# Kernel optimization log

Hardware: AMD Instinct MI355X
Metric: run time of the kernel (lower is better)

## Reference

```python
import jax, jax.numpy as jnp
import numpy as np
from jax import lax

B, T, D = 256, 512, 256          # batch, time, input_dim (neurons)
HE, HC, HG = 256, 256, 256       # encoder/controller/generator hidden
L, F = 64, 64                    # latent_dim, factor_dim


def gru_cell(x, h, Wih, Whh, bih, bhh):
    # PyTorch GRU gate order: r, z, n
    gi = x @ Wih.T + bih
    gh = h @ Whh.T + bhh
    ir, iz, inn = jnp.split(gi, 3, axis=-1)
    hr, hz, hn = jnp.split(gh, 3, axis=-1)
    r = jax.nn.sigmoid(ir + hr)
    z = jax.nn.sigmoid(iz + hz)
    n = jnp.tanh(inn + r * hn)
    return (1.0 - z) * n + z * h


def setup_inputs() -> dict:
    key = jax.random.key(0)
    ks = iter(jax.random.split(key, 40))
    def p(shape, scale=0.05):
        return (jax.random.normal(next(ks), shape, dtype=jnp.float32) * scale)
    inp = {
        "x": jax.random.normal(next(ks), (B, T, D), dtype=jnp.float32),
        "eps_u": jax.random.normal(next(ks), (T, B, L), dtype=jnp.float32),
        # bidirectional encoder GRU (forward / backward directions)
        "Wih_ef": p((3 * HE, D)), "Whh_ef": p((3 * HE, HE)), "bih_ef": p((3 * HE,)), "bhh_ef": p((3 * HE,)),
        "Wih_eb": p((3 * HE, D)), "Whh_eb": p((3 * HE, HE)), "bih_eb": p((3 * HE,)), "bhh_eb": p((3 * HE,)),
        # initial-condition heads
        "W_mu0": p((L, 2 * HE)), "b_mu0": p((L,)), "W_lv0": p((L, 2 * HE)), "b_lv0": p((L,)),
        # controller GRU + heads
        "Wih_c": p((3 * HC, D + F)), "Whh_c": p((3 * HC, HC)), "bih_c": p((3 * HC,)), "bhh_c": p((3 * HC,)),
        "W_cmu": p((L, HC)), "b_cmu": p((L,)), "W_clv": p((L, HC)), "b_clv": p((L,)),
        # generator GRU
        "Wih_g": p((3 * HG, L)), "Whh_g": p((3 * HG, HG)), "bih_g": p((3 * HG,)), "bhh_g": p((3 * HG,)),
        # readouts
        "W_f": p((F, HG)), "b_f": p((F,)), "W_r": p((D, F)), "b_r": p((D,)),
    }
    return inp


def reference(x, eps_u, Wih_ef, Whh_ef, bih_ef, bhh_ef, Wih_eb, Whh_eb, bih_eb, bhh_eb,
              W_mu0, b_mu0, W_lv0, b_lv0, Wih_c, Whh_c, bih_c, bhh_c,
              W_cmu, b_cmu, W_clv, b_clv, Wih_g, Whh_g, bih_g, bhh_g,
              W_f, b_f, W_r, b_r):
    xt = jnp.transpose(x, (1, 0, 2))  # [T, B, D]
    h0 = jnp.zeros((x.shape[0], HE), dtype=x.dtype)

    def enc_f(h, x_t):
        return gru_cell(x_t, h, Wih_ef, Whh_ef, bih_ef, bhh_ef), None

    def enc_b(h, x_t):
        return gru_cell(x_t, h, Wih_eb, Whh_eb, bih_eb, bhh_eb), None

    h_fwd, _ = lax.scan(enc_f, h0, xt)
    h_bwd, _ = lax.scan(enc_b, h0, xt, reverse=True)
    h_enc = jnp.concatenate([h_fwd, h_bwd], axis=-1)  # [B, 2*HE]

    mu0 = h_enc @ W_mu0.T + b_mu0
    lv0 = h_enc @ W_lv0.T + b_lv0
    kl_ics = (0.5 * jnp.sum(jnp.exp(lv0) + mu0 ** 2 - 1.0 - lv0, axis=1)).mean()
    # note: z0 is sampled in the original but never used (generator starts from zeros)

    c0 = jnp.zeros((x.shape[0], HC), dtype=x.dtype)
    g0 = jnp.zeros((x.shape[0], HG), dtype=x.dtype)
    f0 = jnp.zeros((x.shape[0], F), dtype=x.dtype)

    def step(carry, inputs):
        c_h, g_h, prev_f = carry
        x_t, eps_t = inputs
        c_in = jnp.concatenate([x_t, prev_f], axis=-1)  # [B, D+F]
        c_h = gru_cell(c_in, c_h, Wih_c, Whh_c, bih_c, bhh_c)
        mu_u = c_h @ W_cmu.T + b_cmu
        lv_u = c_h @ W_clv.T + b_clv
        u_t = mu_u + eps_t * jnp.exp(0.5 * lv_u)
        kl_t = (0.5 * jnp.sum(jnp.exp(lv_u) + mu_u ** 2 - 1.0 - lv_u, axis=1)).mean()
        g_h = gru_cell(u_t, g_h, Wih_g, Whh_g, bih_g, bhh_g)
        factors = g_h @ W_f.T + b_f
        rates_t = jnp.exp(factors @ W_r.T + b_r)
        return (c_h, g_h, factors), (rates_t, factors, kl_t)

    _, (rates, factors_all, kl_ts) = lax.scan(step, (c0, g0, f0), (xt, eps_u))
    rates = jnp.transpose(rates, (1, 0, 2))           # [B, T, D]
    factors_all = jnp.transpose(factors_all, (1, 0, 2))  # [B, T, F]
    kl_ctrl = kl_ts.mean()  # sum of per-step means / T
    return (rates, kl_ics, kl_ctrl, factors_all)
```

## Files before the change

### kernel.cpp

```cpp
#include <hip/hip_runtime.h>

typedef unsigned char u8;
typedef unsigned short u16;
typedef unsigned int u32;
typedef unsigned long long u64;
typedef short short8 __attribute__((ext_vector_type(8)));
typedef __bf16 bf16x8 __attribute__((ext_vector_type(8)));
typedef float f32x4 __attribute__((ext_vector_type(4)));
typedef float f32x2 __attribute__((ext_vector_type(2)));
typedef long longx2 __attribute__((ext_vector_type(2)));

#define DEV static __device__ __forceinline__

struct Params {
  const float *x, *eps;
  const float *Wih_ef, *Whh_ef, *bih_ef, *bhh_ef;
  const float *Wih_eb, *Whh_eb, *bih_eb, *bhh_eb;
  const float *W_mu0, *b_mu0, *W_lv0, *b_lv0;
  const float *Wih_c, *Whh_c, *bih_c, *bhh_c;
  const float *W_cmu, *b_cmu, *W_clv, *b_clv;
  const float *Wih_g, *Whh_g, *bih_g, *bhh_g;
  const float *W_f, *b_f, *W_r, *b_r;
  u8  *Xf8;
  u16 *ebf;
  u16 *wihcbf;
  float *bfc;
  u8 *wihef8, *whhef8, *wiheb8, *whheb8;
  u8 *whhc8, *whhg8;
  u8 *wihcf8, *wihg8;
  u8 *wf8, *wcmu8, *wclv8;
  u16 *wrbf;
  float *cbn;
  float *gb;
  float *hdb;
  float *fb2;
  float *eb;
  float *henc;
  float *klacc;
  float *klics;
  u8 *Gxc;
  float *out;
};

constexpr size_t RATES_N = 33554432ull;
constexpr size_t FOUT    = RATES_N + 2ull;

DEV u16 f2bf(float x) {
  unsigned u = __builtin_bit_cast(unsigned, x);
  u = (u + 0x7FFFu + ((u >> 16) & 1u)) >> 16;
  return (u16)u;
}
DEV float bf2f(u32 s) { return __builtin_bit_cast(float, s << 16); }
DEV unsigned f2e4m3(float x) {
  unsigned u = __builtin_bit_cast(unsigned, x);
  unsigned s = (u >> 24) & 0x80u;
  float ax = __builtin_bit_cast(float, u & 0x7FFFFFFFu);
  if (ax > 448.f) return s | 0x7E;
  if (ax < 0.0009765625f) return s;
  if (ax < 0.015625f) {
    int m = (int)rintf(ax * 512.f);
    if (m >= 8) return s | 0x08;
    return s | (unsigned)m;
  }
  unsigned au = __builtin_bit_cast(unsigned, ax);
  int E = (int)(au >> 23) - 127;
  unsigned m = au & 0x7FFFFFu;
  unsigned r = (m + 0x7FFFFu + ((m >> 20) & 1u)) >> 20;
  if (r >= 8) { r = 0; ++E; if (E > 8) return s | 0x7E; }
  return s | ((unsigned)(E + 7) << 3) | r;
}
DEV float e4m3tof(unsigned b) {
  unsigned s = (b & 0x80u) << 24;
  unsigned e = (b >> 3) & 15u, m = b & 7u;
  float v;
  if (e) v = __builtin_bit_cast(float, ((e + 120u) << 23) | (m << 20));
  else   v = (float)m * 0.001953125f;
  return __builtin_bit_cast(float, __builtin_bit_cast(unsigned, v) | s);
}
template <bool HI>
DEV unsigned pk2fp8(float a, float b, unsigned old) {
#if __has_builtin(__builtin_amdgcn_cvt_pk_fp8_f32)
  return (unsigned)__builtin_amdgcn_cvt_pk_fp8_f32(a, b, (int)old, HI);
#else
  unsigned p = f2e4m3(a) | (f2e4m3(b) << 8);
  return HI ? ((old & 0xFFFFu) | (p << 16)) : ((old & 0xFFFF0000u) | p);
#endif
}
template <bool HI>
DEV f32x2 pkf32(unsigned w) {
#if __has_builtin(__builtin_amdgcn_cvt_pk_f32_fp8)
  return __builtin_amdgcn_cvt_pk_f32_fp8((int)w, HI);
#else
  unsigned h = HI ? (w >> 16) : w;
  f32x2 r; r[0] = e4m3tof(h & 255u); r[1] = e4m3tof((h >> 8) & 255u); return r;
#endif
}
DEV float sigm(float x) { return 1.f / (1.f + __expf(-x)); }
DEV float ftanh(float x) { float t = __expf(2.f * x); return 1.f - 2.f / (t + 1.f); }
DEV float gru_h(float pr, float pz, float pin, float phn, float hp) {
  float r = sigm(pr), z = sigm(pz);
  float n = ftanh(pin + r * phn);
  return (1.f - z) * n + z * hp;
}
DEV u64 pack8f8(const float* s) {
  u64 p = 0;
  #pragma unroll
  for (int e = 0; e < 8; ++e) p |= (u64)f2e4m3(s[e]) << (8 * e);
  return p;
}

DEV f32x4 MFMA(short8 a, short8 b, f32x4 c) {
  return __builtin_amdgcn_mfma_f32_16x16x32_bf16(
      __builtin_bit_cast(bf16x8, a), __builtin_bit_cast(bf16x8, b), c, 0, 0, 0);
}
DEV f32x4 mfma8(long a, long b, f32x4 c) {
  return __builtin_amdgcn_mfma_f32_16x16x32_fp8_fp8(a, b, c, 0, 0, 0);
}
DEV short8 ldfrag(const u16* p0, int stride) {
  const int l = threadIdx.x & 63;
  const u16* p = p0 + (size_t)(l & 15) * stride + ((l >> 4) << 3);
  return *reinterpret_cast<const short8*>(p);
}
DEV short8 ldfrag_f32(const float* p0, int stride) {
  const int l = threadIdx.x & 63;
  const float* p = p0 + (size_t)(l & 15) * stride + ((l >> 4) << 3);
  f32x4 a = *reinterpret_cast<const f32x4*>(p);
  f32x4 b = *reinterpret_cast<const f32x4*>(p + 4);
  short8 r;
  r[0]=(short)f2bf(a[0]); r[1]=(short)f2bf(a[1]); r[2]=(short)f2bf(a[2]); r[3]=(short)f2bf(a[3]);
  r[4]=(short)f2bf(b[0]); r[5]=(short)f2bf(b[1]); r[6]=(short)f2bf(b[2]); r[7]=(short)f2bf(b[3]);
  return r;
}
DEV longx2 ldws2(const u8* w, int tile, int p) {
  return *(const longx2*)(w + ((size_t)tile << 12) + (p << 10) + ((threadIdx.x & 63) << 4));
}
DEV longx2 ldws64x(const u8* w, int tile) {
  return *(const longx2*)(w + ((size_t)tile << 10) + ((threadIdx.x & 63) << 4));
}
DEV int fragoff(int row, int jb) { return jb * 128 + ((row ^ (jb & 15)) << 3); }
DEV long ldsF(const u8* m, int r0, int rs, int kk) {
  int l = threadIdx.x & 63;
  int jb = kk * 4 + (l >> 4);
  return *(const long*)(m + ((r0 >> 4) << (rs + 4)) + fragoff(l & 15, jb));
}
DEV void stF(u8* m, int row, int col, unsigned v) {
  *(unsigned*)(m + fragoff(row, col >> 3) + (col & 7)) = v;
}
DEV short8 ldsB16(const u8* m, int r0, int kk) {
  int l = threadIdx.x & 63;
  int row = r0 + (l & 15);
  int off = row * 512 + kk * 64 + ((l >> 4) << 4);
  off ^= (row & 7) << 4;
  return *(const short8*)(m + off);
}
DEV void stage16(u8* dst, const u8* src, int nbytes) {
  for (int i = threadIdx.x * 16; i < nbytes; i += blockDim.x * 16) {
    int row = i >> 9;
    int off = i ^ ((row & 7) << 4);
    *(f32x4*)(dst + off) = *(const f32x4*)(src + i);
  }
}

__global__ __launch_bounds__(256) void k_init(Params P) {
  const size_t g  = (size_t)blockIdx.x * 256 + threadIdx.x;
  const size_t gs = (size_t)gridDim.x * 256;
  for (size_t i = g; i < 4194304ull; i += gs) {
    size_t flat = i << 3;
    int b = (int)(flat >> 17);
    int rem = (int)(flat & 131071);
    int t = rem >> 8, d = rem & 255;
    *(u64*)(P.Xf8 + (((size_t)t * 256 + b) << 8) + d) = pack8f8(P.x + flat);
  }
  for (size_t o = g; o < 1048576ull; o += gs) {
    int l = (int)(o & 63), k2 = (int)((o >> 6) & 1);
    int bt = (int)((o >> 7) & 15), t = (int)(o >> 11);
    int row = bt * 16 + (l & 15), col = k2 * 32 + ((l >> 4) << 3);
    const float* s = P.eps + ((size_t)t * 256 + row) * 64 + col;
    f32x4 v0 = *(const f32x4*)s, v1 = *(const f32x4*)(s + 4);
    short8 ob;
    ob[0]=(short)f2bf(v0[0]); ob[1]=(short)f2bf(v0[1]); ob[2]=(short)f2bf(v0[2]); ob[3]=(short)f2bf(v0[3]);
    ob[4]=(short)f2bf(v1[0]); ob[5]=(short)f2bf(v1[1]); ob[6]=(short)f2bf(v1[2]); ob[7]=(short)f2bf(v1[3]);
    *(short8*)((u8*)P.ebf + o * 16) = ob;
  }
  const int gi = (int)g, gsi = (int)gs;
  for (int i = gi; i < 24576; i += gsi) {
    int l = i & 63, kk = (i >> 6) & 7, tile = i >> 9;
    int row = tile * 16 + (l & 15), col = kk * 32 + ((l >> 4) << 3);
    size_t so = (size_t)row * 256 + col;
    size_t db = ((size_t)tile << 12) + ((kk >> 1) << 10) + (l << 4) + ((kk & 1) << 3);
    *(u64*)(P.whhc8  + db) = pack8f8(P.Whh_c  + so);
    *(u64*)(P.whhg8  + db) = pack8f8(P.Whh_g  + so);
    *(u64*)(P.wihef8 + db) = pack8f8(P.Wih_ef + so);
    *(u64*)(P.whhef8 + db) = pack8f8(P.Whh_ef + so);
    *(u64*)(P.wiheb8 + db) = pack8f8(P.Wih_eb + so);
    *(u64*)(P.whheb8 + db) = pack8f8(P.Whh_eb + so);
  }
  for (int i = gi; i < 2048; i += gsi) {
    int l = i & 63, kk = (i >> 6) & 7, tile = i >> 9;
    int row = tile * 16 + (l & 15), col = kk * 32 + ((l >> 4) << 3);
    size_t so = (size_t)row * 256 + col;
    size_t db = ((size_t)tile << 12) + ((kk >> 1) << 10) + (l << 4) + ((kk & 1) << 3);
    *(u64*)(P.wf8   + db) = pack8f8(P.W_f   + so);
    *(u64*)(P.wcmu8 + db) = pack8f8(P.W_cmu + so);
    *(u64*)(P.wclv8 + db) = pack8f8(P.W_clv + so);
  }
  for (int i = gi; i < 6144; i += gsi) {
    int l = i & 63, k2 = (i >> 6) & 1, tile = i >> 7;
    int row = tile * 16 + (l & 15), col = k2 * 32 + ((l >> 4) << 3);
    size_t db = ((size_t)tile << 10) + (l << 4) + (k2 << 3);
    *(u64*)(P.wihcf8 + db) = pack8f8(P.Wih_c + (size_t)row * 320 + 256 + col);
    *(u64*)(P.wihg8  + db) = pack8f8(P.Wih_g + (size_t)row * 64 + col);
  }
  for (int i = gi; i < 196608; i += gsi) {
    int r = i >> 8, c = i & 255;
    P.wihcbf[i] = f2bf(P.Wih_c[r * 320 + c]);
  }
  for (int i = gi; i < 16384; i += gsi) P.wrbf[i] = f2bf(P.W_r[i]);
  for (int i = gi; i < 768; i += gsi)
    P.bfc[i] = P.bih_c[i] + (i < 512 ? P.bhh_c[i] : 0.f);
  for (int i = gi; i < 256; i += gsi) {
    P.cbn[i] = P.bhh_c[512 + i];
    P.gb[i]        = P.bih_g[i] + P.bhh_g[i];
    P.gb[256 + i]  = P.bih_g[256 + i] + P.bhh_g[256 + i];
    P.gb[512 + i]  = P.bih_g[512 + i];
    P.gb[768 + i]  = P.bhh_g[512 + i];
    P.eb[i]        = P.bih_ef[i] + P.bhh_ef[i];
    P.eb[256 + i]  = P.bih_ef[256 + i] + P.bhh_ef[256 + i];
    P.eb[512 + i]  = P.bih_ef[512 + i];
    P.eb[768 + i]  = P.bhh_ef[512 + i];
    P.eb[1024 + i] = P.bih_eb[i] + P.bhh_eb[i];
    P.eb[1280 + i] = P.bih_eb[256 + i] + P.bhh_eb[256 + i];
    P.eb[1536 + i] = P.bih_eb[512 + i];
    P.eb[1792 + i] = P.bhh_eb[512 + i];
  }
  for (int i = gi; i < 128; i += gsi) P.hdb[i] = (i < 64) ? P.b_cmu[i] : P.b_clv[i - 64];
  for (int i = gi; i < 64; i += gsi)  P.fb2[i] = P.b_f[i];
}

__global__ __launch_bounds__(512, 2) void k_gx(Params P) {
  extern __shared__ char smem[];
  u8* sA = (u8*)smem;
  u8* sB = sA + 65536;
  const int nc = blockIdx.x % 6;
  const int tb = blockIdx.x / 6;
  const int t = tb >> 1, bh = tb & 1;
  stage16(sA, (const u8*)(P.wihcbf + (size_t)nc * 128 * 256), 65536);
  for (int i = threadIdx.x * 8; i < 32768; i += 512 * 8) {
    int r = i >> 8, c = i & 255;
    const float* s = P.x + ((size_t)(bh * 128 + r) * 512 + t) * 256 + c;
    f32x4 v0 = *(const f32x4*)s, v1 = *(const f32x4*)(s + 4);
    short8 o;
    o[0]=(short)f2bf(v0[0]); o[1]=(short)f2bf(v0[1]); o[2]=(short)f2bf(v0[2]); o[3]=(short)f2bf(v0[3]);
    o[4]=(short)f2bf(v1[0]); o[5]=(short)f2bf(v1[1]); o[6]=(short)f2bf(v1[2]); o[7]=(short)f2bf(v1[3]);
    int off = (r * 512 + c * 2) ^ ((r & 7) << 4);
    *(short8*)(sB + off) = o;
  }
  __syncthreads();
  const int lane = threadIdx.x & 63, wid = threadIdx.x >> 6;
  const int rq = (lane >> 4) << 2;
  const int nglob = nc * 128 + wid * 16;
  short8 Af[8];
  #pragma unroll
  for (int kk = 0; kk < 8; ++kk) Af[kk] = ldsB16(sA, wid * 16, kk);
  float bq[4];
  #pragma unroll
  for (int q = 0; q < 4; ++q) bq[q] = P.bfc[nglob + rq + q];
  #pragma unroll 1
  for (int bt = 0; bt < 8; ++bt) {
    f32x4 acc = {0.f, 0.f, 0.f, 0.f};
    #pragma unroll
    for (int kk = 0; kk < 8; ++kk)
      acc = MFMA(Af[kk], ldsB16(sB, bt * 16, kk), acc);
    float v0 = acc[0] + bq[0], v1 = acc[1] + bq[1], v2 = acc[2] + bq[2], v3 = acc[3] + bq[3];
    unsigned pw = pk2fp8<false>(v0, v1, 0u); pw = pk2fp8<true>(v2, v3, pw);
    *(u32*)(P.Gxc + (((size_t)(t * 16 + bh * 8 + bt) * 48 + (nglob >> 4)) << 8) + (lane << 2)) = pw;
  }
}

DEV void cg_role(const Params& P, int blk, char* smem) {
  u8* hc8  = (u8*)smem;
  u8* hg8  = hc8 + 8192;
  u8* f8b  = hg8 + 8192;
  float* sml  = (float*)(f8b + 2048);
  float* sred = sml + 16 * 132;

  const int lane = threadIdx.x & 63, wid = threadIdx.x >> 6;
  const int cl = lane & 15, rq = (lane >> 4) << 2;
  const int b0 = blk << 4, j0 = wid << 5, jt = wid << 1;
  const int sel = wid >> 2, l0 = (wid & 3) << 4;

  for (int i = threadIdx.x * 4; i < 18432; i += 512 * 4) *(int*)(hc8 + i) = 0;

  f32x4 bnv[2], brv[2], bzv[2], biv[2], bhv2[2];
  #pragma unroll
  for (int c2 = 0; c2 < 2; ++c2) {
    int j = j0 + c2 * 16 + rq;
    bnv[c2]  = *(const f32x4*)(P.cbn + j);
    brv[c2]  = *(const f32x4*)(P.gb + j);
    bzv[c2]  = *(const f32x4*)(P.gb + 256 + j);
    biv[c2]  = *(const f32x4*)(P.gb + 512 + j);
    bhv2[c2] = *(const f32x4*)(P.gb + 768 + j);
  }
  f32x4 hbv = *(const f32x4*)(P.hdb + sel * 64 + l0 + rq);
  f32x4 fbv = {0, 0, 0, 0};
  if (wid < 4) fbv = *(const f32x4*)(P.fb2 + wid * 16 + rq);

  f32x4 hcM[2] = {{0,0,0,0},{0,0,0,0}};
  f32x4 hgM[2] = {{0,0,0,0},{0,0,0,0}};
  float klv = 0.f;
  __syncthreads();

  #pragma unroll 1
  for (int t = 0; t < 512; ++t) {
    const int cur = t & 1, prv = cur ^ 1;
    u8 *hcP = hc8 + prv * 4096, *hcC = hc8 + cur * 4096;
    u8 *hgP = hg8 + prv * 4096, *hgC = hg8 + cur * 4096;
    int zz = 0; asm volatile("" : "+v"(zz));
    const u8* wcS = P.whhc8 + zz;
    const u8* wgS = P.whhg8 + zz;
    const u8* cfS = P.wihcf8 + zz;
    const u8* guS = P.wihg8 + zz;
    const u8* hdS = (sel ? P.wclv8 : P.wcmu8) + zz;
    const u8* wfS = P.wf8 + zz;
    u32 gx[6];
    { const u8* gp = P.Gxc + (((size_t)(t * 16 + blk) * 48) << 8) + (lane << 2);
      #pragma unroll
      for (int c2 = 0; c2 < 2; ++c2)
        #pragma unroll
        for (int g3 = 0; g3 < 3; ++g3)
          gx[c2 * 3 + g3] = *(const u32*)(gp + ((g3 * 16 + jt + c2) << 8));
    }
    short8 ee0 = *(const short8*)((const u8*)P.ebf + (((size_t)(t * 16 + blk) * 2 + 0) << 10) + lane * 16);
    short8 ee1 = *(const short8*)((const u8*)P.ebf + (((size_t)(t * 16 + blk) * 2 + 1) << 10) + lane * 16);
    long hf[8];
    #pragma unroll
    for (int kk = 0; kk < 8; ++kk) hf[kk] = ldsF(hcP, 0, 8, kk);
    long ff0 = ldsF(f8b + prv * 1024, 0, 6, 0);
    long ff1 = ldsF(f8b + prv * 1024, 0, 6, 1);
    #pragma unroll
    for (int c2 = 0; c2 < 2; ++c2) {
      longx2 w0[4], w1[4], w2[4];
      #pragma unroll
      for (int p = 0; p < 4; ++p) {
        w0[p] = ldws2(wcS,      jt + c2, p);
        w1[p] = ldws2(wcS, 16 + jt + c2, p);
        w2[p] = ldws2(wcS, 32 + jt + c2, p);
      }
      longx2 cf0 = ldws64x(cfS,      jt + c2);
      longx2 cf1 = ldws64x(cfS, 16 + jt + c2);
      longx2 cf2 = ldws64x(cfS, 32 + jt + c2);
      f32x4 ar = {0,0,0,0}, az = {0,0,0,0}, ai = {0,0,0,0}, ah = {0,0,0,0};
      #pragma unroll
      for (int p = 0; p < 4; ++p) {
        ar = mfma8(w0[p].x, hf[2*p], ar);  ar = mfma8(w0[p].y, hf[2*p+1], ar);
        az = mfma8(w1[p].x, hf[2*p], az);  az = mfma8(w1[p].y, hf[2*p+1], az);
        ah = mfma8(w2[p].x, hf[2*p], ah);  ah = mfma8(w2[p].y, hf[2*p+1], ah);
      }
      ar = mfma8(cf0.x, ff0, ar); ar = mfma8(cf0.y, ff1, ar);
      az = mfma8(cf1.x, ff0, az); az = mfma8(cf1.y, ff1, az);
      ai = mfma8(cf2.x, ff0, ai); ai = mfma8(cf2.y, ff1, ai);
      f32x2 rlo = pkf32<false>(gx[c2*3+0]), rhi = pkf32<true>(gx[c2*3+0]);
      f32x2 zlo = pkf32<false>(gx[c2*3+1]), zhi = pkf32<true>(gx[c2*3+1]);
      f32x2 nlo = pkf32<false>(gx[c2*3+2]), nhi = pkf32<true>(gx[c2*3+2]);
      f32x4 bn = bnv[c2];
      float h0 = gru_h(ar[0]+rlo[0], az[0]+zlo[0], ai[0]+nlo[0], ah[0]+bn[0], hcM[c2][0]);
      float h1 = gru_h(ar[1]+rlo[1], az[1]+zlo[1], ai[1]+nlo[1], ah[1]+bn[1], hcM[c2][1]);
      float h2 = gru_h(ar[2]+rhi[0], az[2]+zhi[0], ai[2]+nhi[0], ah[2]+bn[2], hcM[c2][2]);
      float h3 = gru_h(ar[3]+rhi[1], az[3]+zhi[1], ai[3]+nhi[1], ah[3]+bn[3], hcM[c2][3]);
      hcM[c2][0] = h0; hcM[c2][1] = h1; hcM[c2][2] = h2; hcM[c2][3] = h3;
      unsigned pw = pk2fp8<false>(h0, h1, 0u); pw = pk2fp8<true>(h2, h3, pw);
      stF(hcC, cl, j0 + c2 * 16 + rq, pw);
    }
    __syncthreads();
    { long hcv[8];
      #pragma unroll
      for (int kk = 0; kk < 8; ++kk) hcv[kk] = ldsF(hcC, 0, 8, kk);
      f32x4 am = {0,0,0,0};
      #pragma unroll
      for (int p = 0; p < 4; ++p) {
        longx2 wp = ldws2(hdS, wid & 3, p);
        am = mfma8(wp.x, hcv[2*p], am);
        am = mfma8(wp.y, hcv[2*p+1], am);
      }
      am += hbv;
      *(f32x4*)(sml + cl * 132 + sel * 64 + l0 + rq) = am;
    }
    __syncthreads();
    long U[2];
    { const float* ml = sml + cl * 132;
      const int kh = (lane >> 4) << 3;
      #pragma unroll
      for (int k2 = 0; k2 < 2; ++k2) {
        f32x4 mu0 = *(const f32x4*)(ml + k2 * 32 + kh);
        f32x4 mu1 = *(const f32x4*)(ml + k2 * 32 + kh + 4);
        f32x4 lv0 = *(const f32x4*)(ml + 64 + k2 * 32 + kh);
        f32x4 lv1 = *(const f32x4*)(ml + 64 + k2 * 32 + kh + 4);
        short8 ev = k2 ? ee1 : ee0;
        float uu[8];
        #pragma unroll
        for (int e = 0; e < 4; ++e) {
          float epv = bf2f((u32)(u16)ev[e]);
          uu[e] = mu0[e] + epv * __expf(0.5f * lv0[e]);
        }
        #pragma unroll
        for (int e = 0; e < 4; ++e) {
          float epv = bf2f((u32)(u16)ev[4 + e]);
          uu[4 + e] = mu1[e] + epv * __expf(0.5f * lv1[e]);
        }
        unsigned pa = pk2fp8<false>(uu[0], uu[1], 0u); pa = pk2fp8<true>(uu[2], uu[3], pa);
        unsigned pb = pk2fp8<false>(uu[4], uu[5], 0u); pb = pk2fp8<true>(uu[6], uu[7], pb);
        U[k2] = (long)(((u64)pb << 32) | (u64)pa);
      }
    }
    long hg[8];
    #pragma unroll
    for (int kk = 0; kk < 8; ++kk) hg[kk] = ldsF(hgP, 0, 8, kk);
    #pragma unroll
    for (int c2 = 0; c2 < 2; ++c2) {
      longx2 g0[4], g1[4], g2[4];
      #pragma unroll
      for (int p = 0; p < 4; ++p) {
        g0[p] = ldws2(wgS,      jt + c2, p);
        g1[p] = ldws2(wgS, 16 + jt + c2, p);
        g2[p] = ldws2(wgS, 32 + jt + c2, p);
      }
      longx2 u0 = ldws64x(guS,      jt + c2);
      longx2 u1 = ldws64x(guS, 16 + jt + c2);
      longx2 u2 = ldws64x(guS, 32 + jt + c2);
      f32x4 gr = {0,0,0,0}, gz = {0,0,0,0}, gi = {0,0,0,0}, gh = {0,0,0,0};
      #pragma unroll
      for (int p = 0; p < 4; ++p) {
        gr = mfma8(g0[p].x, hg[2*p], gr);  gr = mfma8(g0[p].y, hg[2*p+1], gr);
        gz = mfma8(g1[p].x, hg[2*p], gz);  gz = mfma8(g1[p].y, hg[2*p+1], gz);
        gh = mfma8(g2[p].x, hg[2*p], gh);  gh = mfma8(g2[p].y, hg[2*p+1], gh);
      }
      gr = mfma8(u0.x, U[0], gr); gr = mfma8(u0.y, U[1], gr);
      gz = mfma8(u1.x, U[0], gz); gz = mfma8(u1.y, U[1], gz);
      gi = mfma8(u2.x, U[0], gi); gi = mfma8(u2.y, U[1], gi);
      float h0 = gru_h(gr[0]+brv[c2][0], gz[0]+bzv[c2][0], gi[0]+biv[c2][0], gh[0]+bhv2[c2][0], hgM[c2][0]);
      float h1 = gru_h(gr[1]+brv[c2][1], gz[1]+bzv[c2][1], gi[1]+biv[c2][1], gh[1]+bhv2[c2][1], hgM[c2][1]);
      float h2 = gru_h(gr[2]+brv[c2][2], gz[2]+bzv[c2][2], gi[2]+biv[c2][2], gh[2]+bhv2[c2][2], hgM[c2][2]);
      float h3 = gru_h(gr[3]+brv[c2][3], gz[3]+bzv[c2][3], gi[3]+biv[c2][3], gh[3]+bhv2[c2][3], hgM[c2][3]);
      hgM[c2][0] = h0; hgM[c2][1] = h1; hgM[c2][2] = h2; hgM[c2][3] = h3;
      unsigned pw = pk2fp8<false>(h0, h1, 0u); pw = pk2fp8<true>(h2, h3, pw);
      stF(hgC, cl, j0 + c2 * 16 + rq, pw);
    }
    __syncthreads();
    if (wid < 4) {
      long hgv[8];
      #pragma unroll
      for (int kk = 0; kk < 8; ++kk) hgv[kk] = ldsF(hgC, 0, 8, kk);
      f32x4 af = {0,0,0,0};
      #pragma unroll
      for (int p = 0; p < 4; ++p) {
        longx2 wp = ldws2(wfS, wid, p);
        af = mfma8(wp.x, hgv[2*p], af);
        af = mfma8(wp.y, hgv[2*p+1], af);
      }
      af += fbv;
      float* fo = P.out + FOUT + (size_t)(b0 + cl) * 32768 + (size_t)t * 64 + wid * 16 + rq;
      f32x2 lo = {af[0], af[1]}, hi2 = {af[2], af[3]};
      *(f32x2*)fo = lo;
      *(f32x2*)(fo + 2) = hi2;
      unsigned pw = pk2fp8<false>(af[0], af[1], 0u); pw = pk2fp8<true>(af[2], af[3], pw);
      stF(f8b + cur * 1024, cl, wid * 16 + rq, pw);
    } else {
      #pragma unroll
      for (int e = 0; e < 4; ++e) {
        int p = ((wid - 4) * 64 + lane) * 4 + e;
        int row = p >> 6, l = p & 63;
        float mu = sml[row * 132 + l], lv = sml[row * 132 + 64 + l];
        klv += __expf(lv) + mu * mu - 1.f - lv;
      }
    }
    __syncthreads();
  }
  if (wid >= 4) {
    float v = klv;
    v += __shfl_down(v, 32); v += __shfl_down(v, 16); v += __shfl_down(v, 8);
    v += __shfl_down(v, 4);  v += __shfl_down(v, 2);  v += __shfl_down(v, 1);
    if (lane == 0) sred[wid] = v;
  }
  __syncthreads();
  if (threadIdx.x == 0) P.klacc[blk] = sred[4] + sred[5] + sred[6] + sred[7];
}

DEV void enc_role(const Params& P, int dir, int b0, char* smem) {
  u8* h8 = (u8*)smem;
  u8* sx = h8 + 8192;
  const int lane = threadIdx.x & 63, wid = threadIdx.x >> 6;
  const int cl = lane & 15, rq = (lane >> 4) << 2;
  const int j0 = wid << 5, jt = wid << 1;
  const u8* wihS0 = dir ? P.wiheb8 : P.wihef8;
  const u8* whhS0 = dir ? P.whheb8 : P.whhef8;
  const float* ebt = P.eb + dir * 1024;
  for (int i = threadIdx.x * 4; i < 8192; i += 512 * 4) *(int*)(h8 + i) = 0;
  f32x4 brv[2], bzv[2], biv[2], bhv2[2];
  #pragma unroll
  for (int c2 = 0; c2 < 2; ++c2) {
    int j = j0 + c2 * 16 + rq;
    brv[c2]  = *(const f32x4*)(ebt + j);
    bzv[c2]  = *(const f32x4*)(ebt + 256 + j);
    biv[c2]  = *(const f32x4*)(ebt + 512 + j);
    bhv2[c2] = *(const f32x4*)(ebt + 768 + j);
  }
  f32x4 heM[2] = {{0,0,0,0},{0,0,0,0}};
  const int ssrc = threadIdx.x * 8;
  const int sdst = fragoff(threadIdx.x >> 5, threadIdx.x & 31);
  const int t0 = dir ? 511 : 0;
  *(u64*)(sx + sdst) = *(const u64*)(P.Xf8 + (((size_t)t0 * 256 + b0) << 8) + ssrc);
  __syncthreads();

  #pragma unroll 1
  for (int i = 0; i < 512; ++i) {
    const int cur = i & 1, prv = cur ^ 1;
    const int t = dir ? (511 - i) : i;
    u8 *hP = h8 + prv * 4096, *hC = h8 + cur * 4096;
    const u8* sxc = sx + cur * 4096;
    int zz = 0; asm volatile("" : "+v"(zz));
    const u8* wihS = wihS0 + zz;
    const u8* whhS = whhS0 + zz;
    u64 xpre = 0;
    if (i < 511) {
      int tn = dir ? (t - 1) : (t + 1);
      xpre = *(const u64*)(P.Xf8 + (((size_t)tn * 256 + b0) << 8) + ssrc);
    }
    long hp[8], xv[8];
    #pragma unroll
    for (int kk = 0; kk < 8; ++kk) { hp[kk] = ldsF(hP, 0, 8, kk); xv[kk] = ldsF(sxc, 0, 8, kk); }
    #pragma unroll
    for (int c2 = 0; c2 < 2; ++c2) {
      longx2 H0[4], H1[4], H2[4], I0[4], I1[4], I2[4];
      #pragma unroll
      for (int p = 0; p < 4; ++p) {
        H0[p] = ldws2(whhS,      jt + c2, p);
        H1[p] = ldws2(whhS, 16 + jt + c2, p);
        H2[p] = ldws2(whhS, 32 + jt + c2, p);
        I0[p] = ldws2(wihS,      jt + c2, p);
        I1[p] = ldws2(wihS, 16 + jt + c2, p);
        I2[p] = ldws2(wihS, 32 + jt + c2, p);
      }
      f32x4 er = {0,0,0,0}, ez = {0,0,0,0}, ei = {0,0,0,0}, eh = {0,0,0,0};
      #pragma unroll
      for (int p = 0; p < 4; ++p) {
        er = mfma8(H0[p].x, hp[2*p], er);  er = mfma8(H0[p].y, hp[2*p+1], er);
        ez = mfma8(H1[p].x, hp[2*p], ez);  ez = mfma8(H1[p].y, hp[2*p+1], ez);
        eh = mfma8(H2[p].x, hp[2*p], eh);  eh = mfma8(H2[p].y, hp[2*p+1], eh);
        er = mfma8(I0[p].x, xv[2*p], er);  er = mfma8(I0[p].y, xv[2*p+1], er);
        ez = mfma8(I1[p].x, xv[2*p], ez);  ez = mfma8(I1[p].y, xv[2*p+1], ez);
        ei = mfma8(I2[p].x, xv[2*p], ei);  ei = mfma8(I2[p].y, xv[2*p+1], ei);
      }
      float h0 = gru_h(er[0]+brv[c2][0], ez[0]+bzv[c2][0], ei[0]+biv[c2][0], eh[0]+bhv2[c2][0], heM[c2][0]);
      float h1 = gru_h(er[1]+brv[c2][1], ez[1]+bzv[c2][1], ei[1]+biv[c2][1], eh[1]+bhv2[c2][1], heM[c2][1]);
      float h2 = gru_h(er[2]+brv[c2][2], ez[2]+bzv[c2][2], ei[2]+biv[c2][2], eh[2]+bhv2[c2][2], heM[c2][2]);
      float h3 = gru_h(er[3]+brv[c2][3], ez[3]+bzv[c2][3], ei[3]+biv[c2][3], eh[3]+bhv2[c2][3], heM[c2][3]);
      heM[c2][0] = h0; heM[c2][1] = h1; heM[c2][2] = h2; heM[c2][3] = h3;
      unsigned pw = pk2fp8<false>(h0, h1, 0u); pw = pk2fp8<true>(h2, h3, pw);
      stF(hC, cl, j0 + c2 * 16 + rq, pw);
    }
    if (i < 511) *(u64*)(sx + prv * 4096 + sdst) = xpre;
    __syncthreads();
  }
  #pragma unroll
  for (int c2 = 0; c2 < 2; ++c2)
    *(f32x4*)(P.henc + (size_t)(dir * 256 + b0 + cl) * 256 + j0 + c2 * 16 + rq) = heM[c2];
}

__global__ __launch_bounds__(512, 2) void k_main(Params P) {
  extern __shared__ char smem[];
  const int blk = blockIdx.x;
  if (blk < 16) cg_role(P, blk, smem);
  else {
    const int e = blk - 16;
    enc_role(P, e >> 4, (e & 15) << 4, smem);
  }
}

__global__ __launch_bounds__(256) void k_post(Params P) {
  const int blk = blockIdx.x;
  if (blk < 32) {
    __shared__ float red[4];
    float ka = 0.f;
    #pragma unroll 1
    for (int pp = 0; pp < 2; ++pp) {
      int p = blk * 512 + threadIdx.x * 2 + pp;
      int b = p >> 6, l = p & 63;
      float mu = P.b_mu0[l], lv = P.b_lv0[l];
      const float* wm = P.W_mu0 + (size_t)l * 512;
      const float* wl = P.W_lv0 + (size_t)l * 512;
      const float* h0 = P.henc + (size_t)b * 256;
      const float* h1 = P.henc + (size_t)(256 + b) * 256;
      #pragma unroll 4
      for (int k = 0; k < 256; ++k) {
        float hf = h0[k], hb = h1[k];
        mu += hf * wm[k] + hb * wm[256 + k];
        lv += hf * wl[k] + hb * wl[256 + k];
      }
      ka += __expf(lv) + mu * mu - 1.f - lv;
    }
    const int lane = threadIdx.x & 63, wid = threadIdx.x >> 6;
    ka += __shfl_down(ka, 32); ka += __shfl_down(ka, 16); ka += __shfl_down(ka, 8);
    ka += __shfl_down(ka, 4);  ka += __shfl_down(ka, 2);  ka += __shfl_down(ka, 1);
    if (lane == 0) red[wid] = ka;
    __syncthreads();
    if (threadIdx.x == 0) P.klics[blk] = red[0] + red[1] + red[2] + red[3];
  } else {
    const int lane = threadIdx.x & 63, wid = threadIdx.x >> 6;
    const int cl = lane & 15, rq = (lane >> 4) << 2;
    const int gw = (blk - 32) * 4 + wid;
    const size_t r0 = (size_t)gw << 4;
    const float* Fs = P.out + FOUT;
    short8 F0 = ldfrag_f32(Fs + r0 * 64, 64);
    short8 F1 = ldfrag_f32(Fs + r0 * 64 + 32, 64);
    #pragma unroll 1
    for (int ct = 0; ct < 16; ++ct) {
      const int d0 = ct << 4;
      const u16* W = P.wrbf + (size_t)d0 * 64;
      f32x4 a = {0,0,0,0};
      a = MFMA(ldfrag(W, 64), F0, a);
      a = MFMA(ldfrag(W + 32, 64), F1, a);
      f32x4 rb = *(const f32x4*)(P.b_r + d0 + rq);
      f32x4 o;
      o[0] = __expf(a[0] + rb[0]); o[1] = __expf(a[1] + rb[1]);
      o[2] = __expf(a[2] + rb[2]); o[3] = __expf(a[3] + rb[3]);
      *(f32x4*)(P.out + (r0 + cl) * 256 + d0 + rq) = o;
    }
  }
}

__global__ void k_final(Params P) {
  if (threadIdx.x == 0) {
    float s = 0.f, s2 = 0.f;
    for (int i = 0; i < 16; ++i) s += P.klacc[i];
    for (int i = 0; i < 32; ++i) s2 += P.klics[i];
    P.out[RATES_N]     = s2 * (0.5f / 256.f);
    P.out[RATES_N + 1] = s  * (0.5f / (256.f * 512.f));
  }
}

extern "C" void kernel_launch(void* const* d_in, const int* in_sizes, int n_in,
                              void* d_out, int out_size, void* d_ws, size_t ws_size,
                              hipStream_t stream) {
  (void)in_sizes; (void)n_in; (void)out_size; (void)ws_size;
  Params P;
  const float* const* in = (const float* const*)d_in;
  P.x = in[0];      P.eps = in[1];
  P.Wih_ef = in[2]; P.Whh_ef = in[3]; P.bih_ef = in[4]; P.bhh_ef = in[5];
  P.Wih_eb = in[6]; P.Whh_eb = in[7]; P.bih_eb = in[8]; P.bhh_eb = in[9];
  P.W_mu0 = in[10]; P.b_mu0 = in[11]; P.W_lv0 = in[12]; P.b_lv0 = in[13];
  P.Wih_c = in[14]; P.Whh_c = in[15]; P.bih_c = in[16]; P.bhh_c = in[17];
  P.W_cmu = in[18]; P.b_cmu = in[19]; P.W_clv = in[20]; P.b_clv = in[21];
  P.Wih_g = in[22]; P.Whh_g = in[23]; P.bih_g = in[24]; P.bhh_g = in[25];
  P.W_f = in[26];   P.b_f = in[27];   P.W_r = in[28];   P.b_r = in[29];

  char* w = (char*)d_ws;
  size_t off = 0;
  auto take = [&](size_t bytes) -> char* {
    char* r = w + off;
    off = (off + bytes + 255) & ~(size_t)255;
    return r;
  };
  P.Xf8    = (u8*)take(33554432ull);
  P.ebf    = (u16*)take(16777216ull * 2);
  P.wihcbf = (u16*)take(196608ull * 2);
  P.bfc    = (float*)take(768ull * 4);
  P.wihef8 = (u8*)take(196608ull);
  P.whhef8 = (u8*)take(196608ull);
  P.wiheb8 = (u8*)take(196608ull);
  P.whheb8 = (u8*)take(196608ull);
  P.whhc8  = (u8*)take(196608ull);
  P.whhg8  = (u8*)take(196608ull);
  P.wihcf8 = (u8*)take(49152ull);
  P.wihg8  = (u8*)take(49152ull);
  P.wf8    = (u8*)take(16384ull);
  P.wcmu8  = (u8*)take(16384ull);
  P.wclv8  = (u8*)take(16384ull);
  P.wrbf   = (u16*)take(16384ull * 2);
  P.cbn    = (float*)take(256ull * 4);
  P.gb     = (float*)take(1024ull * 4);
  P.hdb    = (float*)take(128ull * 4);
  P.fb2    = (float*)take(64ull * 4);
  P.eb     = (float*)take(2048ull * 4);
  P.henc   = (float*)take(131072ull * 4);
  P.klacc  = (float*)take(64ull * 4);
  P.klics  = (float*)take(64ull * 4);
  P.Gxc    = (u8*)d_out;
  P.out    = (float*)d_out;

  hipLaunchKernelGGL(k_init,  dim3(2048), dim3(256), 0, stream, P);
  hipLaunchKernelGGL(k_gx,    dim3(6144), dim3(512), 131072, stream, P);
  hipLaunchKernelGGL(k_main,  dim3(48),   dim3(512), 27008, stream, P);
  hipLaunchKernelGGL(k_post,  dim3(2080), dim3(256), 0, stream, P);
  hipLaunchKernelGGL(k_final, dim3(1),    dim3(64),  0, stream, P);
}
```

Before: 4.712 ms.

## Double wave count in recurrent kernel so each wave owns one 16-column tile

```diff
diff --git a/kernel.cpp b/kernel.cpp
--- a/kernel.cpp
+++ b/kernel.cpp
@@ -286,27 +286,23 @@
 
   const int lane = threadIdx.x & 63, wid = threadIdx.x >> 6;
   const int cl = lane & 15, rq = (lane >> 4) << 2;
-  const int b0 = blk << 4, j0 = wid << 5, jt = wid << 1;
-  const int sel = wid >> 2, l0 = (wid & 3) << 4;
-
-  for (int i = threadIdx.x * 4; i < 18432; i += 512 * 4) *(int*)(hc8 + i) = 0;
-
-  f32x4 bnv[2], brv[2], bzv[2], biv[2], bhv2[2];
-  #pragma unroll
-  for (int c2 = 0; c2 < 2; ++c2) {
-    int j = j0 + c2 * 16 + rq;
-    bnv[c2]  = *(const f32x4*)(P.cbn + j);
-    brv[c2]  = *(const f32x4*)(P.gb + j);
-    bzv[c2]  = *(const f32x4*)(P.gb + 256 + j);
-    biv[c2]  = *(const f32x4*)(P.gb + 512 + j);
-    bhv2[c2] = *(const f32x4*)(P.gb + 768 + j);
-  }
-  f32x4 hbv = *(const f32x4*)(P.hdb + sel * 64 + l0 + rq);
-  f32x4 fbv = {0, 0, 0, 0};
-  if (wid < 4) fbv = *(const f32x4*)(P.fb2 + wid * 16 + rq);
-
-  f32x4 hcM[2] = {{0,0,0,0},{0,0,0,0}};
-  f32x4 hgM[2] = {{0,0,0,0},{0,0,0,0}};
+  const int b0 = blk << 4, j0 = wid << 4;
+
+  for (int i = threadIdx.x * 4; i < 18432; i += 1024 * 4) *(int*)(hc8 + i) = 0;
+
+  f32x4 bnv, brv, bzv, biv, bhv2;
+  { int j = j0 + rq;
+    bnv  = *(const f32x4*)(P.cbn + j);
+    brv  = *(const f32x4*)(P.gb + j);
+    bzv  = *(const f32x4*)(P.gb + 256 + j);
+    biv  = *(const f32x4*)(P.gb + 512 + j);
+    bhv2 = *(const f32x4*)(P.gb + 768 + j);
+  }
+  f32x4 hbv = {0,0,0,0}, fbv = {0,0,0,0};
+  if (wid < 8) hbv = *(const f32x4*)(P.hdb + ((wid >> 2) & 1) * 64 + ((wid & 3) << 4) + rq);
+  if (wid < 4) fbv = *(const f32x4*)(P.fb2 + (wid << 4) + rq);
+
+  f32x4 hcM = {0,0,0,0}, hgM = {0,0,0,0};
   float klv = 0.f;
   __syncthreads();
 
@@ -320,15 +316,12 @@
     const u8* wgS = P.whhg8 + zz;
     const u8* cfS = P.wihcf8 + zz;
     const u8* guS = P.wihg8 + zz;
-    const u8* hdS = (sel ? P.wclv8 : P.wcmu8) + zz;
     const u8* wfS = P.wf8 + zz;
-    u32 gx[6];
+    u32 gx0, gx1, gx2;
     { const u8* gp = P.Gxc + (((size_t)(t * 16 + blk) * 48) << 8) + (lane << 2);
-      #pragma unroll
-      for (int c2 = 0; c2 < 2; ++c2)
-        #pragma unroll
-        for (int g3 = 0; g3 < 3; ++g3)
-          gx[c2 * 3 + g3] = *(const u32*)(gp + ((g3 * 16 + jt + c2) << 8));
+      gx0 = *(const u32*)(gp + ((0 * 16 + wid) << 8));
+      gx1 = *(const u32*)(gp + ((1 * 16 + wid) << 8));
+      gx2 = *(const u32*)(gp + ((2 * 16 + wid) << 8));
     }
     short8 ee0 = *(const short8*)((const u8*)P.ebf + (((size_t)(t * 16 + blk) * 2 + 0) << 10) + lane * 16);
     short8 ee1 = *(const short8*)((const u8*)P.ebf + (((size_t)(t * 16 + blk) * 2 + 1) << 10) + lane * 16);
@@ -337,18 +330,17 @@
     for (int kk = 0; kk < 8; ++kk) hf[kk] = ldsF(hcP, 0, 8, kk);
     long ff0 = ldsF(f8b + prv * 1024, 0, 6, 0);
     long ff1 = ldsF(f8b + prv * 1024, 0, 6, 1);
-    #pragma unroll
-    for (int c2 = 0; c2 < 2; ++c2) {
+    {
       longx2 w0[4], w1[4], w2[4];
       #pragma unroll
       for (int p = 0; p < 4; ++p) {
-        w0[p] = ldws2(wcS,      jt + c2, p);
-        w1[p] = ldws2(wcS, 16 + jt + c2, p);
-        w2[p] = ldws2(wcS, 32 + jt + c2, p);
-      }
-      longx2 cf0 = ldws64x(cfS,      jt + c2);
-      longx2 cf1 = ldws64x(cfS, 16 + jt + c2);
-      longx2 cf2 = ldws64x(cfS, 32 + jt + c2);
+        w0[p] = ldws2(wcS,      wid, p);
+        w1[p] = ldws2(wcS, 16 + wid, p);
+        w2[p] = ldws2(wcS, 32 + wid, p);
+      }
+      longx2 cf0 = ldws64x(cfS,      wid);
+      longx2 cf1 = ldws64x(cfS, 16 + wid);
+      longx2 cf2 = ldws64x(cfS, 32 + wid);
       f32x4 ar = {0,0,0,0}, az = {0,0,0,0}, ai = {0,0,0,0}, ah = {0,0,0,0};
       #pragma unroll
       for (int p = 0; p < 4; ++p) {
@@ -359,20 +351,22 @@
       ar = mfma8(cf0.x, ff0, ar); ar = mfma8(cf0.y, ff1, ar);
       az = mfma8(cf1.x, ff0, az); az = mfma8(cf1.y, ff1, az);
       ai = mfma8(cf2.x, ff0, ai); ai = mfma8(cf2.y, ff1, ai);
-      f32x2 rlo = pkf32<false>(gx[c2*3+0]), rhi = pkf32<true>(gx[c2*3+0]);
-      f32x2 zlo = pkf32<false>(gx[c2*3+1]), zhi = pkf32<true>(gx[c2*3+1]);
-      f32x2 nlo = pkf32<false>(gx[c2*3+2]), nhi = pkf32<true>(gx[c2*3+2]);
-      f32x4 bn = bnv[c2];
-      float h0 = gru_h(ar[0]+rlo[0], az[0]+zlo[0], ai[0]+nlo[0], ah[0]+bn[0], hcM[c2][0]);
-      float h1 = gru_h(ar[1]+rlo[1], az[1]+zlo[1], ai[1]+nlo[1], ah[1]+bn[1], hcM[c2][1]);
-      float h2 = gru_h(ar[2]+rhi[0], az[2]+zhi[0], ai[2]+nhi[0], ah[2]+bn[2], hcM[c2][2]);
-      float h3 = gru_h(ar[3]+rhi[1], az[3]+zhi[1], ai[3]+nhi[1], ah[3]+bn[3], hcM[c2][3]);
-      hcM[c2][0] = h0; hcM[c2][1] = h1; hcM[c2][2] = h2; hcM[c2][3] = h3;
+      f32x2 rlo = pkf32<false>(gx0), rhi = pkf32<true>(gx0);
+      f32x2 zlo = pkf32<false>(gx1), zhi = pkf32<true>(gx1);
+      f32x2 nlo = pkf32<false>(gx2), nhi = pkf32<true>(gx2);
+      float h0 = gru_h(ar[0]+rlo[0], az[0]+zlo[0], ai[0]+nlo[0], ah[0]+bnv[0], hcM[0]);
+      float h1 = gru_h(ar[1]+rlo[1], az[1]+zlo[1], ai[1]+nlo[1], ah[1]+bnv[1], hcM[1]);
+      float h2 = gru_h(ar[2]+rhi[0], az[2]+zhi[0], ai[2]+nhi[0], ah[2]+bnv[2], hcM[2]);
+      float h3 = gru_h(ar[3]+rhi[1], az[3]+zhi[1], ai[3]+nhi[1], ah[3]+bnv[3], hcM[3]);
+      hcM[0] = h0; hcM[1] = h1; hcM[2] = h2; hcM[3] = h3;
       unsigned pw = pk2fp8<false>(h0, h1, 0u); pw = pk2fp8<true>(h2, h3, pw);
-      stF(hcC, cl, j0 + c2 * 16 + rq, pw);
+      stF(hcC, cl, j0 + rq, pw);
     }
     __syncthreads();
-    { long hcv[8];
+    if (wid < 8) {
+      const int sel = (wid >> 2) & 1, l0 = (wid & 3) << 4;
+      const u8* hdS = (sel ? P.wclv8 : P.wcmu8) + zz;
+      long hcv[8];
       #pragma unroll
       for (int kk = 0; kk < 8; ++kk) hcv[kk] = ldsF(hcC, 0, 8, kk);
       f32x4 am = {0,0,0,0};
@@ -415,18 +409,17 @@
     long hg[8];
     #pragma unroll
     for (int kk = 0; kk < 8; ++kk) hg[kk] = ldsF(hgP, 0, 8, kk);
-    #pragma unroll
-    for (int c2 = 0; c2 < 2; ++c2) {
+    {
       longx2 g0[4], g1[4], g2[4];
       #pragma unroll
       for (int p = 0; p < 4; ++p) {
-        g0[p] = ldws2(wgS,      jt + c2, p);
-        g1[p] = ldws2(wgS, 16 + jt + c2, p);
-        g2[p] = ldws2(wgS, 32 + jt + c2, p);
-      }
-      longx2 u0 = ldws64x(guS,      jt + c2);
-      longx2 u1 = ldws64x(guS, 16 + jt + c2);
-      longx2 u2 = ldws64x(guS, 32 + jt + c2);
+        g0[p] = ldws2(wgS,      wid, p);
+        g1[p] = ldws2(wgS, 16 + wid, p);
+        g2[p] = ldws2(wgS, 32 + wid, p);
+      }
+      longx2 u0 = ldws64x(guS,      wid);
+      longx2 u1 = ldws64x(guS, 16 + wid);
+      longx2 u2 = ldws64x(guS, 32 + wid);
       f32x4 gr = {0,0,0,0}, gz = {0,0,0,0}, gi = {0,0,0,0}, gh = {0,0,0,0};
       #pragma unroll
       for (int p = 0; p < 4; ++p) {
@@ -437,13 +430,13 @@
       gr = mfma8(u0.x, U[0], gr); gr = mfma8(u0.y, U[1], gr);
       gz = mfma8(u1.x, U[0], gz); gz = mfma8(u1.y, U[1], gz);
       gi = mfma8(u2.x, U[0], gi); gi = mfma8(u2.y, U[1], gi);
-      float h0 = gru_h(gr[0]+brv[c2][0], gz[0]+bzv[c2][0], gi[0]+biv[c2][0], gh[0]+bhv2[c2][0], hgM[c2][0]);
-      float h1 = gru_h(gr[1]+brv[c2][1], gz[1]+bzv[c2][1], gi[1]+biv[c2][1], gh[1]+bhv2[c2][1], hgM[c2][1]);
-      float h2 = gru_h(gr[2]+brv[c2][2], gz[2]+bzv[c2][2], gi[2]+biv[c2][2], gh[2]+bhv2[c2][2], hgM[c2][2]);
-      float h3 = gru_h(gr[3]+brv[c2][3], gz[3]+bzv[c2][3], gi[3]+biv[c2][3], gh[3]+bhv2[c2][3], hgM[c2][3]);
-      hgM[c2][0] = h0; hgM[c2][1] = h1; hgM[c2][2] = h2; hgM[c2][3] = h3;
+      float h0 = gru_h(gr[0]+brv[0], gz[0]+bzv[0], gi[0]+biv[0], gh[0]+bhv2[0], hgM[0]);
+      float h1 = gru_h(gr[1]+brv[1], gz[1]+bzv[1], gi[1]+biv[1], gh[1]+bhv2[1], hgM[1]);
+      float h2 = gru_h(gr[2]+brv[2], gz[2]+bzv[2], gi[2]+biv[2], gh[2]+bhv2[2], hgM[2]);
+      float h3 = gru_h(gr[3]+brv[3], gz[3]+bzv[3], gi[3]+biv[3], gh[3]+bhv2[3], hgM[3]);
+      hgM[0] = h0; hgM[1] = h1; hgM[2] = h2; hgM[3] = h3;
       unsigned pw = pk2fp8<false>(h0, h1, 0u); pw = pk2fp8<true>(h2, h3, pw);
-      stF(hgC, cl, j0 + c2 * 16 + rq, pw);
+      stF(hgC, cl, j0 + rq, pw);
     }
     __syncthreads();
     if (wid < 4) {
@@ -464,10 +457,10 @@
       *(f32x2*)(fo + 2) = hi2;
       unsigned pw = pk2fp8<false>(af[0], af[1], 0u); pw = pk2fp8<true>(af[2], af[3], pw);
       stF(f8b + cur * 1024, cl, wid * 16 + rq, pw);
-    } else {
-      #pragma unroll
-      for (int e = 0; e < 4; ++e) {
-        int p = ((wid - 4) * 64 + lane) * 4 + e;
+    } else if (wid >= 8) {
+      #pragma unroll
+      for (int e = 0; e < 2; ++e) {
+        int p = ((wid - 8) * 64 + lane) * 2 + e;
         int row = p >> 6, l = p & 63;
         float mu = sml[row * 132 + l], lv = sml[row * 132 + 64 + l];
         klv += __expf(lv) + mu * mu - 1.f - lv;
@@ -475,14 +468,19 @@
     }
     __syncthreads();
   }
-  if (wid >= 4) {
+  if (wid >= 8) {
     float v = klv;
     v += __shfl_down(v, 32); v += __shfl_down(v, 16); v += __shfl_down(v, 8);
     v += __shfl_down(v, 4);  v += __shfl_down(v, 2);  v += __shfl_down(v, 1);
     if (lane == 0) sred[wid] = v;
   }
   __syncthreads();
-  if (threadIdx.x == 0) P.klacc[blk] = sred[4] + sred[5] + sred[6] + sred[7];
+  if (threadIdx.x == 0) {
+    float s = 0.f;
+    #pragma unroll
+    for (int i = 8; i < 16; ++i) s += sred[i];
+    P.klacc[blk] = s;
+  }
 }
 
 DEV void enc_role(const Params& P, int dir, int b0, char* smem) {
@@ -490,25 +488,25 @@
   u8* sx = h8 + 8192;
   const int lane = threadIdx.x & 63, wid = threadIdx.x >> 6;
   const int cl = lane & 15, rq = (lane >> 4) << 2;
-  const int j0 = wid << 5, jt = wid << 1;
+  const int j0 = wid << 4;
   const u8* wihS0 = dir ? P.wiheb8 : P.wihef8;
   const u8* whhS0 = dir ? P.whheb8 : P.whhef8;
   const float* ebt = P.eb + dir * 1024;
-  for (int i = threadIdx.x * 4; i < 8192; i += 512 * 4) *(int*)(h8 + i) = 0;
-  f32x4 brv[2], bzv[2], biv[2], bhv2[2];
-  #pragma unroll
-  for (int c2 = 0; c2 < 2; ++c2) {
-    int j = j0 + c2 * 16 + rq;
-    brv[c2]  = *(const f32x4*)(ebt + j);
-    bzv[c2]  = *(const f32x4*)(ebt + 256 + j);
-    biv[c2]  = *(const f32x4*)(ebt + 512 + j);
-    bhv2[c2] = *(const f32x4*)(ebt + 768 + j);
-  }
-  f32x4 heM[2] = {{0,0,0,0},{0,0,0,0}};
-  const int ssrc = threadIdx.x * 8;
-  const int sdst = fragoff(threadIdx.x >> 5, threadIdx.x & 31);
+  for (int i = threadIdx.x * 4; i < 8192; i += 1024 * 4) *(int*)(h8 + i) = 0;
+  f32x4 brv, bzv, biv, bhv2;
+  { int j = j0 + rq;
+    brv  = *(const f32x4*)(ebt + j);
+    bzv  = *(const f32x4*)(ebt + 256 + j);
+    biv  = *(const f32x4*)(ebt + 512 + j);
+    bhv2 = *(const f32x4*)(ebt + 768 + j);
+  }
+  f32x4 heM = {0,0,0,0};
+  const int su = threadIdx.x;
+  const int sr = su >> 6, sk = (su & 63) * 4;
+  const int ssrc = sr * 256 + sk;
+  const int sdst = fragoff(sr, sk >> 3) + (sk & 7);
   const int t0 = dir ? 511 : 0;
-  *(u64*)(sx + sdst) = *(const u64*)(P.Xf8 + (((size_t)t0 * 256 + b0) << 8) + ssrc);
+  *(u32*)(sx + sdst) = *(const u32*)(P.Xf8 + (((size_t)t0 * 256 + b0) << 8) + ssrc);
   __syncthreads();
 
   #pragma unroll 1
@@ -520,53 +518,59 @@
     int zz = 0; asm volatile("" : "+v"(zz));
     const u8* wihS = wihS0 + zz;
     const u8* whhS = whhS0 + zz;
-    u64 xpre = 0;
+    u32 xpre = 0;
     if (i < 511) {
       int tn = dir ? (t - 1) : (t + 1);
-      xpre = *(const u64*)(P.Xf8 + (((size_t)tn * 256 + b0) << 8) + ssrc);
+      xpre = *(const u32*)(P.Xf8 + (((size_t)tn * 256 + b0) << 8) + ssrc);
     }
     long hp[8], xv[8];
     #pragma unroll
     for (int kk = 0; kk < 8; ++kk) { hp[kk] = ldsF(hP, 0, 8, kk); xv[kk] = ldsF(sxc, 0, 8, kk); }
-    #pragma unroll
-    for (int c2 = 0; c2 < 2; ++c2) {
-      longx2 H0[4], H1[4], H2[4], I0[4], I1[4], I2[4];
-      #pragma unroll
-      for (int p = 0; p < 4; ++p) {
-        H0[p] = ldws2(whhS,      jt + c2, p);
-        H1[p] = ldws2(whhS, 16 + jt + c2, p);
-        H2[p] = ldws2(whhS, 32 + jt + c2, p);
-        I0[p] = ldws2(wihS,      jt + c2, p);
-        I1[p] = ldws2(wihS, 16 + jt + c2, p);
-        I2[p] = ldws2(wihS, 32 + jt + c2, p);
-      }
-      f32x4 er = {0,0,0,0}, ez = {0,0,0,0}, ei = {0,0,0,0}, eh = {0,0,0,0};
+    f32x4 er = {0,0,0,0}, ez = {0,0,0,0}, ei = {0,0,0,0}, eh = {0,0,0,0};
+    {
+      longx2 H0[4], H1[4], H2[4];
+      #pragma unroll
+      for (int p = 0; p < 4; ++p) {
+        H0[p] = ldws2(whhS,      wid, p);
+        H1[p] = ldws2(whhS, 16 + wid, p);
+        H2[p] = ldws2(whhS, 32 + wid, p);
+      }
       #pragma unroll
       for (int p = 0; p < 4; ++p) {
         er = mfma8(H0[p].x, hp[2*p], er);  er = mfma8(H0[p].y, hp[2*p+1], er);
         ez = mfma8(H1[p].x, hp[2*p], ez);  ez = mfma8(H1[p].y, hp[2*p+1], ez);
         eh = mfma8(H2[p].x, hp[2*p], eh);  eh = mfma8(H2[p].y, hp[2*p+1], eh);
+      }
+    }
+    {
+      longx2 I0[4], I1[4], I2[4];
+      #pragma unroll
+      for (int p = 0; p < 4; ++p) {
+        I0[p] = ldws2(wihS,      wid, p);
+        I1[p] = ldws2(wihS, 16 + wid, p);
+        I2[p] = ldws2(wihS, 32 + wid, p);
+      }
+      #pragma unroll
+      for (int p = 0; p < 4; ++p) {
         er = mfma8(I0[p].x, xv[2*p], er);  er = mfma8(I0[p].y, xv[2*p+1], er);
         ez = mfma8(I1[p].x, xv[2*p], ez);  ez = mfma8(I1[p].y, xv[2*p+1], ez);
         ei = mfma8(I2[p].x, xv[2*p], ei);  ei = mfma8(I2[p].y, xv[2*p+1], ei);
       }
-      float h0 = gru_h(er[0]+brv[c2][0], ez[0]+bzv[c2][0], ei[0]+biv[c2][0], eh[0]+bhv2[c2][0], heM[c2][0]);
-      float h1 = gru_h(er[1]+brv[c2][1], ez[1]+bzv[c2][1], ei[1]+biv[c2][1], eh[1]+bhv2[c2][1], heM[c2][1]);
-      float h2 = gru_h(er[2]+brv[c2][2], ez[2]+bzv[c2][2], ei[2]+biv[c2][2], eh[2]+bhv2[c2][2], heM[c2][2]);
-      float h3 = gru_h(er[3]+brv[c2][3], ez[3]+bzv[c2][3], ei[3]+biv[c2][3], eh[3]+bhv2[c2][3], heM[c2][3]);
-      heM[c2][0] = h0; heM[c2][1] = h1; heM[c2][2] = h2; heM[c2][3] = h3;
-      unsigned pw = pk2fp8<false>(h0, h1, 0u); pw = pk2fp8<true>(h2, h3, pw);
-      stF(hC, cl, j0 + c2 * 16 + rq, pw);
-    }
-    if (i < 511) *(u64*)(sx + prv * 4096 + sdst) = xpre;
+    }
+    float h0 = gru_h(er[0]+brv[0], ez[0]+bzv[0], ei[0]+biv[0], eh[0]+bhv2[0], heM[0]);
+    float h1 = gru_h(er[1]+brv[1], ez[1]+bzv[1], ei[1]+biv[1], eh[1]+bhv2[1], heM[1]);
+    float h2 = gru_h(er[2]+brv[2], ez[2]+bzv[2], ei[2]+biv[2], eh[2]+bhv2[2], heM[2]);
+    float h3 = gru_h(er[3]+brv[3], ez[3]+bzv[3], ei[3]+biv[3], eh[3]+bhv2[3], heM[3]);
+    heM[0] = h0; heM[1] = h1; heM[2] = h2; heM[3] = h3;
+    unsigned pw = pk2fp8<false>(h0, h1, 0u); pw = pk2fp8<true>(h2, h3, pw);
+    stF(hC, cl, j0 + rq, pw);
+    if (i < 511) *(u32*)(sx + prv * 4096 + sdst) = xpre;
     __syncthreads();
   }
-  #pragma unroll
-  for (int c2 = 0; c2 < 2; ++c2)
-    *(f32x4*)(P.henc + (size_t)(dir * 256 + b0 + cl) * 256 + j0 + c2 * 16 + rq) = heM[c2];
-}
-
-__global__ __launch_bounds__(512, 2) void k_main(Params P) {
+  *(f32x4*)(P.henc + (size_t)(dir * 256 + b0 + cl) * 256 + j0 + rq) = heM;
+}
+
+__global__ __launch_bounds__(1024) void k_main(Params P) {
   extern __shared__ char smem[];
   const int blk = blockIdx.x;
   if (blk < 16) cg_role(P, blk, smem);
@@ -689,7 +693,7 @@
 
   hipLaunchKernelGGL(k_init,  dim3(2048), dim3(256), 0, stream, P);
   hipLaunchKernelGGL(k_gx,    dim3(6144), dim3(512), 131072, stream, P);
-  hipLaunchKernelGGL(k_main,  dim3(48),   dim3(512), 27008, stream, P);
+  hipLaunchKernelGGL(k_main,  dim3(48),   dim3(1024), 27008, stream, P);
   hipLaunchKernelGGL(k_post,  dim3(2080), dim3(256), 0, stream, P);
   hipLaunchKernelGGL(k_final, dim3(1),    dim3(64),  0, stream, P);
 }
```

Result: slower. 6.355 ms (+34.9%).
